# Kernel optimization log

Measured on AMD Instinct MI355X. Metric: run time of the kernel, lower is better.

## Reference

```python
import jax, jax.numpy as jnp
import numpy as np

N, M, DIM = 50000, 800000, 64
EPS_MSG = 1e-7
BN_EPS = 1e-5


def setup_inputs() -> dict:
    key = jax.random.key(0)
    ks = jax.random.split(key, 12)
    x = jax.random.normal(ks[0], (N, DIM), dtype=jnp.float32)
    edge_index = jax.random.randint(ks[1], (2, M), 0, N, dtype=jnp.int64)
    edge_attr = jax.random.normal(ks[2], (M, DIM), dtype=jnp.float32)
    s = 1.0 / np.sqrt(DIM)
    s2 = 1.0 / np.sqrt(2 * DIM)
    # 3 GENConv layers, each with MLP: Linear(dim,2dim)->BN->ReLU->Linear(2dim,dim)
    W1 = jax.random.uniform(ks[3], (3, DIM, 2 * DIM), jnp.float32, -s, s)
    b1 = jax.random.uniform(ks[4], (3, 2 * DIM), jnp.float32, -s, s)
    gamma = jnp.ones((3, 2 * DIM), jnp.float32)
    beta = jnp.zeros((3, 2 * DIM), jnp.float32)
    W2 = jax.random.uniform(ks[5], (3, 2 * DIM, DIM), jnp.float32, -s2, s2)
    b2 = jax.random.uniform(ks[6], (3, DIM), jnp.float32, -s2, s2)
    return {"x": x, "edge_index": edge_index, "edge_attr": edge_attr,
            "W1": W1, "b1": b1, "gamma": gamma, "beta": beta, "W2": W2, "b2": b2}


def _genconv(x, src, dst, edge_attr, W1, b1, g, be, W2, b2):
    n = x.shape[0]
    # message: relu(x_j + e) + eps   (per-edge)
    msg = jax.nn.relu(x[src] + edge_attr) + EPS_MSG  # [M, dim]
    # softmax aggregation (per-destination, per-channel), t=1.0
    mx = jax.ops.segment_max(msg, dst, num_segments=n)
    mx = jnp.where(jnp.isfinite(mx), mx, 0.0)  # empty segments
    e = jnp.exp(msg - mx[dst])
    ssum = jax.ops.segment_sum(e, dst, num_segments=n)
    alpha = e / jnp.maximum(ssum[dst], 1e-16)
    agg = jax.ops.segment_sum(msg * alpha, dst, num_segments=n)  # [N, dim]
    # residual then MLP: Linear -> BatchNorm(train) -> ReLU -> Linear
    h = agg + x
    h1 = h @ W1 + b1
    mu = h1.mean(axis=0)
    var = h1.var(axis=0)
    h1 = (h1 - mu) * jax.lax.rsqrt(var + BN_EPS) * g + be
    h1 = jax.nn.relu(h1)
    return h1 @ W2 + b2


def reference(x, edge_index, edge_attr, W1, b1, gamma, beta, W2, b2):
    src, dst = edge_index[0], edge_index[1]
    for i in range(3):
        x = _genconv(x, src, dst, edge_attr, W1[i], b1[i], gamma[i], beta[i], W2[i], b2[i])
    return x
```

## Files before the change

kernel.cpp:

```cpp
#include <hip/hip_runtime.h>
#include <hip/hip_fp16.h>

#define DIM 64
#define D2  128


__global__ void k_detect(const int* __restrict__ ei, int m, int* __restrict__ flag) {
  __shared__ int nz;
  int t = threadIdx.x;
  if (t == 0) nz = 0;
  __syncthreads();
  int lim = 4096;
  if (lim > m / 2) lim = m / 2;
  int any = 0;
  for (int i = t; i < lim; i += 256) any |= (ei[2 * i + 1] != 0);
  if (any) atomicOr(&nz, 1);
  __syncthreads();
  if (t == 0) flag[0] = nz ? 0 : 1;
}

__global__ void k_hist(const int* __restrict__ ei, int m, const int* __restrict__ flag,
                       int* __restrict__ cnt) {
  int i = blockIdx.x * 256 + threadIdx.x;
  if (i >= m) return;
  int f = flag[0];
  int d = f ? ei[2 * ((size_t)m + i)] : ei[(size_t)m + i];
  atomicAdd(&cnt[d], 1);
}

__global__ void k_scanA(const int* __restrict__ cnt, int* __restrict__ excl,
                        int* __restrict__ bsum, int n) {
  __shared__ int lds[256];
  int t = threadIdx.x;
  int i = blockIdx.x * 256 + t;
  int v = (i < n) ? cnt[i] : 0;
  lds[t] = v;
  __syncthreads();
  for (int off = 1; off < 256; off <<= 1) {
    int u = (t >= off) ? lds[t - off] : 0;
    __syncthreads();
    lds[t] += u;
    __syncthreads();
  }
  if (i < n) excl[i] = lds[t] - v;
  if (t == 255) bsum[blockIdx.x] = lds[255];
}

__global__ void k_scanC(const int* __restrict__ excl, const int* __restrict__ bsum,
                        int* __restrict__ start, int* __restrict__ cursor, int n, int m) {
  __shared__ int red[256];
  __shared__ int boffS;
  int t = threadIdx.x;
  int acc = 0;
  for (int i = t; i < blockIdx.x; i += 256) acc += bsum[i];
  red[t] = acc;
  __syncthreads();
  for (int off = 128; off > 0; off >>= 1) {
    if (t < off) red[t] += red[t + off];
    __syncthreads();
  }
  if (t == 0) boffS = red[0];
  __syncthreads();
  int i = blockIdx.x * 256 + t;
  if (i < n) {
    int s = excl[i] + boffS;
    start[i] = s;
    cursor[i] = s;
  }
  if (blockIdx.x == 0 && t == 0) start[n] = m;
}

__global__ void k_scatter(const int* __restrict__ ei, int m, const int* __restrict__ flag,
                          int* __restrict__ cursor, int2* __restrict__ sed) {
  int i = blockIdx.x * 256 + threadIdx.x;
  if (i >= m) return;
  int f = flag[0];
  int s, d;
  if (f) { s = ei[2 * (size_t)i]; d = ei[2 * ((size_t)m + i)]; }
  else   { s = ei[i];             d = ei[(size_t)m + i]; }
  int pos = atomicAdd(&cursor[d], 1);
  sed[pos] = make_int2(i, s);
}

__global__ __launch_bounds__(256) void k_canon(
    int2* __restrict__ sed, const int* __restrict__ start, int n) {
  int lane = threadIdx.x & 63;
  int node = blockIdx.x * 4 + (threadIdx.x >> 6);
  if (node >= n) return;
  int s0 = start[node], s1 = start[node + 1];

#define BSTEP(K, J)                                   \
  {                                                   \
    int o = __shfl_xor(key, (J), 64);                 \
    bool dir = ((lane & (K)) == 0);                   \
    bool lo = ((lane & (J)) == 0);                    \
    int mn = key < o ? key : o;                       \
    int mx = key < o ? o : key;                       \
    key = (dir == lo) ? mn : mx;                      \
  }

  for (int base = s0; base < s1; base += 64) {
    int cnt = s1 - base;
    if (cnt > 64) cnt = 64;
    int key = 0x7fffffff;
    int srcReg = 0;
    if (lane < cnt) {
      int2 e = sed[base + lane];
      key = (e.x << 6) | lane;
      srcReg = e.y;
    }
#pragma unroll
    for (int k = 2; k <= 16; k <<= 1) {
#pragma unroll
      for (int j = k >> 1; j > 0; j >>= 1) BSTEP(k, j)
    }
    if (cnt > 16) {
#pragma unroll
      for (int j = 16; j > 0; j >>= 1) BSTEP(32, j)
      if (cnt > 32) {
#pragma unroll
        for (int j = 32; j > 0; j >>= 1) BSTEP(64, j)
      }
    }
    int org = key & 63;
    int eid = (int)(((unsigned)key) >> 6);
    int src = __shfl(srcReg, org, 64);
    if (lane < cnt) sed[base + lane] = make_int2(eid, src);
  }
#undef BSTEP
}

__global__ __launch_bounds__(256) void k_perm(
    const float* __restrict__ ea, const int2* __restrict__ sed,
    __half* __restrict__ eah, int m) {
  int cl = threadIdx.x & 15;
  int grp = (blockIdx.x * 256 + threadIdx.x) >> 4;
  int ngrp = (gridDim.x * 256) >> 4;
  for (int p0 = grp * 4; p0 < m; p0 += ngrp * 4) {
#pragma unroll
    for (int k = 0; k < 4; k++) {
      int p = p0 + k;
      if (p < m) {
        int eid = sed[p].x;
        float4 v = *(const float4*)(ea + ((size_t)eid << 6) + (cl << 2));
        __half2 h0 = __floats2half2_rn(v.x, v.y);
        __half2 h1 = __floats2half2_rn(v.z, v.w);
        uint2 u;
        u.x = *(unsigned*)&h0;
        u.y = *(unsigned*)&h1;
        *(uint2*)(eah + (((size_t)p) << 6) + (cl << 2)) = u;
      }
    }
  }
}

__global__ __launch_bounds__(256) void k_agg_s(
    const float* __restrict__ x, const __half* __restrict__ eah,
    const int2* __restrict__ sed, const int* __restrict__ start,
    float* __restrict__ h, int n) {
  int lane = threadIdx.x & 63;
  int node = blockIdx.x * 4 + (threadIdx.x >> 6);
  if (node >= n) return;
  int sub = lane >> 4;
  int cl = lane & 15;
  int s0 = start[node], s1 = start[node + 1];

  float sS[4] = {0.f, 0.f, 0.f, 0.f};
  float wW[4] = {0.f, 0.f, 0.f, 0.f};

#define CONSUME()                                                       \
  {                                                                     \
    float2 a01 = __half22float2(*(const __half2*)&av.x);                \
    float2 a23 = __half22float2(*(const __half2*)&av.y);                \
    float g0 = fmaxf(xv.x + a01.x, 0.f) + 1e-7f;                        \
    float g1 = fmaxf(xv.y + a01.y, 0.f) + 1e-7f;                        \
    float g2 = fmaxf(xv.z + a23.x, 0.f) + 1e-7f;                        \
    float g3 = fmaxf(xv.w + a23.y, 0.f) + 1e-7f;                        \
    float p0 = __expf(g0), p1 = __expf(g1), p2 = __expf(g2), p3 = __expf(g3); \
    sS[0] += p0; sS[1] += p1; sS[2] += p2; sS[3] += p3;                 \
    wW[0] = fmaf(g0, p0, wW[0]); wW[1] = fmaf(g1, p1, wW[1]);           \
    wW[2] = fmaf(g2, p2, wW[2]); wW[3] = fmaf(g3, p3, wW[3]);           \
  }

  for (int base = s0; base < s1; base += 64) {
    int cnt = s1 - base;
    if (cnt > 64) cnt = 64;
    int sK = 0;
    if (lane < cnt) sK = sed[base + lane].y;
    int full = cnt >> 2;
    int rem = cnt & 3;
    int idx = (sub < cnt) ? sub : 0;
    int src = __shfl(sK, idx, 64);
    float4 xv = *(const float4*)(x + ((size_t)src << 6) + (cl << 2));
    uint2 av = *(const uint2*)(eah + (((size_t)(base + idx)) << 6) + (cl << 2));
    for (int t = 0; t < full; t++) {
      int nidx = 4 * t + 4 + sub;
      int nidxc = (nidx < cnt) ? nidx : 0;
      int nsrc = __shfl(sK, nidxc, 64);
      float4 nxv = *(const float4*)(x + ((size_t)nsrc << 6) + (cl << 2));
      uint2 nav = *(const uint2*)(eah + (((size_t)(base + nidxc)) << 6) + (cl << 2));
      CONSUME()
      xv = nxv; av = nav;
    }
    if (rem) {
      if (sub < rem) CONSUME()
    }
  }
#undef CONSUME

#pragma unroll
  for (int off = 16; off < 64; off <<= 1) {
#pragma unroll
    for (int c = 0; c < 4; c++) {
      sS[c] += __shfl_xor(sS[c], off, 64);
      wW[c] += __shfl_xor(wW[c], off, 64);
    }
  }

  if (sub == 0) {
    size_t xo = ((size_t)node << 6) + (cl << 2);
    float4 xv = *(const float4*)(x + xo);
    float4 o;
    o.x = wW[0] / fmaxf(sS[0], 1e-16f) + xv.x;
    o.y = wW[1] / fmaxf(sS[1], 1e-16f) + xv.y;
    o.z = wW[2] / fmaxf(sS[2], 1e-16f) + xv.z;
    o.w = wW[3] / fmaxf(sS[3], 1e-16f) + xv.w;
    *(float4*)(h + xo) = o;
  }
}

__global__ __launch_bounds__(256) void k_agg_g(
    const float* __restrict__ x, const float* __restrict__ ea,
    const int2* __restrict__ sed, const int* __restrict__ start,
    float* __restrict__ h, int n) {
  int lane = threadIdx.x & 63;
  int node = blockIdx.x * 4 + (threadIdx.x >> 6);
  if (node >= n) return;
  int sub = lane >> 4;
  int cl = lane & 15;
  int s0 = start[node], s1 = start[node + 1];

  float sS[4] = {0.f, 0.f, 0.f, 0.f};
  float wW[4] = {0.f, 0.f, 0.f, 0.f};

#define ACC(EID, SRC)                                                   \
  {                                                                     \
    unsigned xo = ((unsigned)(SRC) << 6) + (cl << 2);                   \
    unsigned ao = ((unsigned)(EID) << 6) + (cl << 2);                   \
    float4 xv = *(const float4*)(x + xo);                               \
    float4 av = *(const float4*)(ea + ao);                              \
    float g0 = fmaxf(xv.x + av.x, 0.f) + 1e-7f;                         \
    float g1 = fmaxf(xv.y + av.y, 0.f) + 1e-7f;                         \
    float g2 = fmaxf(xv.z + av.z, 0.f) + 1e-7f;                         \
    float g3 = fmaxf(xv.w + av.w, 0.f) + 1e-7f;                         \
    float p0 = __expf(g0), p1 = __expf(g1), p2 = __expf(g2), p3 = __expf(g3); \
    sS[0] += p0; sS[1] += p1; sS[2] += p2; sS[3] += p3;                 \
    wW[0] = fmaf(g0, p0, wW[0]); wW[1] = fmaf(g1, p1, wW[1]);           \
    wW[2] = fmaf(g2, p2, wW[2]); wW[3] = fmaf(g3, p3, wW[3]);           \
  }

  for (int base = s0; base < s1; base += 64) {
    int cnt = s1 - base;
    if (cnt > 64) cnt = 64;
    int eK = 0, sK = 0;
    if (lane < cnt) {
      int2 e = sed[base + lane];
      eK = e.x; sK = e.y;
    }
    int full = cnt >> 2;
    int rem = cnt & 3;
    for (int t = 0; t < full; t++) {
      int idx = 4 * t + sub;
      int eid = __shfl(eK, idx, 64);
      int src = __shfl(sK, idx, 64);
      ACC(eid, src)
    }
    if (rem) {
      int idx = 4 * full + sub;
      int idxc = idx < cnt ? idx : 0;
      int eid = __shfl(eK, idxc, 64);
      int src = __shfl(sK, idxc, 64);
      if (sub < rem) ACC(eid, src)
    }
  }
#undef ACC

#pragma unroll
  for (int off = 16; off < 64; off <<= 1) {
#pragma unroll
    for (int c = 0; c < 4; c++) {
      sS[c] += __shfl_xor(sS[c], off, 64);
      wW[c] += __shfl_xor(wW[c], off, 64);
    }
  }

  if (sub == 0) {
    unsigned xo = ((unsigned)node << 6) + (cl << 2);
    float4 xv = *(const float4*)(x + xo);
    float4 o;
    o.x = wW[0] / fmaxf(sS[0], 1e-16f) + xv.x;
    o.y = wW[1] / fmaxf(sS[1], 1e-16f) + xv.y;
    o.z = wW[2] / fmaxf(sS[2], 1e-16f) + xv.z;
    o.w = wW[3] / fmaxf(sS[3], 1e-16f) + xv.w;
    *(float4*)(h + xo) = o;
  }
}

__global__ __launch_bounds__(256) void k_gemm1(
    const float* __restrict__ h, const float* __restrict__ W1,
    const float* __restrict__ b1, float* __restrict__ h1,
    float* __restrict__ ps, float* __restrict__ pq, int n) {
  __shared__ float ws[DIM * D2];
  __shared__ float hs[DIM][68];
  __shared__ float red[8][D2];
  int tid = threadIdx.x;
  int row0 = blockIdx.x * 64;
  const float4* w4 = (const float4*)W1;
  float4* ws4 = (float4*)ws;
#pragma unroll
  for (int i = 0; i < 8; i++) ws4[tid + 256 * i] = w4[tid + 256 * i];
  const float4* h4 = (const float4*)h;
#pragma unroll
  for (int i = 0; i < 4; i++) {
    int idx = tid + 256 * i;
    int r = idx & 63, dg = idx >> 6;
    int row = row0 + r;
    float4 v = make_float4(0.f, 0.f, 0.f, 0.f);
    if (row < n) v = h4[(size_t)row * 16 + dg];
    int c = dg * 4;
    hs[c + 0][r] = v.x; hs[c + 1][r] = v.y; hs[c + 2][r] = v.z; hs[c + 3][r] = v.w;
  }
  __syncthreads();

  int tc = tid & 31, tr = tid >> 5;
  float bb[4];
#pragma unroll
  for (int k = 0; k < 4; k++) bb[k] = b1[tc * 4 + k];
  float acc[8][4];
#pragma unroll
  for (int i = 0; i < 8; i++)
#pragma unroll
    for (int k = 0; k < 4; k++) acc[i][k] = bb[k];
#pragma unroll 4
  for (int d = 0; d < DIM; d++) {
    float4 wv = *(const float4*)&ws[d * D2 + tc * 4];
    float4 ha = *(const float4*)&hs[d][tr * 8];
    float4 hb = *(const float4*)&hs[d][tr * 8 + 4];
    float hr[8] = {ha.x, ha.y, ha.z, ha.w, hb.x, hb.y, hb.z, hb.w};
    float wk[4] = {wv.x, wv.y, wv.z, wv.w};
#pragma unroll
    for (int i = 0; i < 8; i++)
#pragma unroll
      for (int k = 0; k < 4; k++) acc[i][k] = fmaf(hr[i], wk[k], acc[i][k]);
  }
  float cs[4] = {0.f, 0.f, 0.f, 0.f}, cq[4] = {0.f, 0.f, 0.f, 0.f};
#pragma unroll
  for (int i = 0; i < 8; i++) {
    int row = row0 + tr * 8 + i;
    if (row < n) {
      ((float4*)h1)[(size_t)row * 32 + tc] =
          make_float4(acc[i][0], acc[i][1], acc[i][2], acc[i][3]);
#pragma unroll
      for (int k = 0; k < 4; k++) { cs[k] += acc[i][k]; cq[k] += acc[i][k] * acc[i][k]; }
    }
  }
  __syncthreads();
#pragma unroll
  for (int k = 0; k < 4; k++) red[tr][tc * 4 + k] = cs[k];
  __syncthreads();
  float asum = 0.f;
  if (tid < D2) {
#pragma unroll
    for (int r = 0; r < 8; r++) asum += red[r][tid];
  }
  __syncthreads();
#pragma unroll
  for (int k = 0; k < 4; k++) red[tr][tc * 4 + k] = cq[k];
  __syncthreads();
  if (tid < D2) {
    float bsumv = 0.f;
#pragma unroll
    for (int r = 0; r < 8; r++) bsumv += red[r][tid];
    ps[(size_t)tid * gridDim.x + blockIdx.x] = asum;
    pq[(size_t)tid * gridDim.x + blockIdx.x] = bsumv;
  }
}

__global__ __launch_bounds__(256) void k_stats(
    const float* __restrict__ ps, const float* __restrict__ pq,
    const float* __restrict__ gamma, const float* __restrict__ beta,
    float* __restrict__ ss, int rows, int n) {
  __shared__ float r0[256], r1[256];
  int j = blockIdx.x;
  int t = threadIdx.x;
  float a = 0.f, b = 0.f;
  for (int r = t; r < rows; r += 256) {
    a += ps[(size_t)j * rows + r];
    b += pq[(size_t)j * rows + r];
  }
  r0[t] = a; r1[t] = b;
  __syncthreads();
  for (int off = 128; off > 0; off >>= 1) {
    if (t < off) { r0[t] += r0[t + off]; r1[t] += r1[t + off]; }
    __syncthreads();
  }
  if (t == 0) {
    float mu = r0[0] / (float)n;
    float var = r1[0] / (float)n - mu * mu;
    float sc = gamma[j] * rsqrtf(var + 1e-5f);
    ss[j] = sc;
    ss[D2 + j] = beta[j] - mu * sc;
  }
}

__global__ __launch_bounds__(256) void k_gemm2(
    const float* __restrict__ h1, const float* __restrict__ W2,
    const float* __restrict__ b2, const float* __restrict__ ss,
    float* __restrict__ out, int n) {
  __shared__ float ws2[D2 * DIM];
  __shared__ float hs[D2][68];
  __shared__ float scS[D2], shS[D2];
  int tid = threadIdx.x;
  int row0 = blockIdx.x * 64;
  const float4* w4 = (const float4*)W2;
  float4* ws4 = (float4*)ws2;
#pragma unroll
  for (int i = 0; i < 8; i++) ws4[tid + 256 * i] = w4[tid + 256 * i];
  if (tid < D2) { scS[tid] = ss[tid]; shS[tid] = ss[D2 + tid]; }
  __syncthreads();
  const float4* h14 = (const float4*)h1;
#pragma unroll
  for (int i = 0; i < 8; i++) {
    int idx = tid + 256 * i;
    int r = idx & 63, cg = idx >> 6;
    int row = row0 + r;
    float4 v = make_float4(0.f, 0.f, 0.f, 0.f);
    if (row < n) v = h14[(size_t)row * 32 + cg];
    int c = cg * 4;
    hs[c + 0][r] = fmaxf(fmaf(v.x, scS[c + 0], shS[c + 0]), 0.f);
    hs[c + 1][r] = fmaxf(fmaf(v.y, scS[c + 1], shS[c + 1]), 0.f);
    hs[c + 2][r] = fmaxf(fmaf(v.z, scS[c + 2], shS[c + 2]), 0.f);
    hs[c + 3][r] = fmaxf(fmaf(v.w, scS[c + 3], shS[c + 3]), 0.f);
  }
  __syncthreads();
  int tc = tid & 15, tr = tid >> 4;
  float bb[4];
#pragma unroll
  for (int k = 0; k < 4; k++) bb[k] = b2[tc * 4 + k];
  float acc[4][4];
#pragma unroll
  for (int i = 0; i < 4; i++)
#pragma unroll
    for (int k = 0; k < 4; k++) acc[i][k] = bb[k];
#pragma unroll 4
  for (int d = 0; d < D2; d++) {
    float4 wv = *(const float4*)&ws2[d * DIM + tc * 4];
    float4 hv = *(const float4*)&hs[d][tr * 4];
    float hr[4] = {hv.x, hv.y, hv.z, hv.w};
    float wk[4] = {wv.x, wv.y, wv.z, wv.w};
#pragma unroll
    for (int i = 0; i < 4; i++)
#pragma unroll
      for (int k = 0; k < 4; k++) acc[i][k] = fmaf(hr[i], wk[k], acc[i][k]);
  }
#pragma unroll
  for (int i = 0; i < 4; i++) {
    int row = row0 + tr * 4 + i;
    if (row < n)
      ((float4*)out)[(size_t)row * 16 + tc] =
          make_float4(acc[i][0], acc[i][1], acc[i][2], acc[i][3]);
  }
}

extern "C" void kernel_launch(void* const* d_in, const int* in_sizes, int n_in,
                              void* d_out, int out_size, void* d_ws, size_t ws_size,
                              hipStream_t stream) {
  (void)n_in; (void)out_size;
  const float* x0    = (const float*)d_in[0];
  const int*   ei    = (const int*)d_in[1];
  const float* ea    = (const float*)d_in[2];
  const float* W1    = (const float*)d_in[3];
  const float* b1    = (const float*)d_in[4];
  const float* gamma = (const float*)d_in[5];
  const float* beta  = (const float*)d_in[6];
  const float* W2    = (const float*)d_in[7];
  const float* b2    = (const float*)d_in[8];
  float* out = (float*)d_out;

  int n = in_sizes[0] / DIM;
  int m = in_sizes[1] / 2;

  char* base = (char*)d_ws;
  size_t off = 0;
  auto alloc = [&](size_t bytes) -> void* {
    void* p = base + off;
    off += (bytes + 255) & ~(size_t)255;
    return p;
  };
  int*    cnt    = (int*)alloc((size_t)n * 4);
  int*    excl   = (int*)alloc((size_t)n * 4);
  int*    bsum   = (int*)alloc(256 * 4);
  int*    start  = (int*)alloc((size_t)(n + 1) * 4);
  int*    cursor = (int*)alloc((size_t)n * 4);
  int*    flag   = (int*)alloc(256);
  int2*   sed    = (int2*)alloc((size_t)m * 8);
  float*  h      = (float*)alloc((size_t)n * DIM * 4);
  float*  h1     = (float*)alloc((size_t)n * D2 * 4);
  int tiles = (n + 63) / 64;
  float* ps = (float*)alloc((size_t)tiles * D2 * 4);
  float* pq = (float*)alloc((size_t)tiles * D2 * 4);
  float* ss = (float*)alloc(256 * 4);
  size_t eah_bytes = (size_t)m * DIM * 2;
  __half* eah = nullptr;
  if (ws_size >= off + eah_bytes) eah = (__half*)alloc(eah_bytes);

  hipMemsetAsync(cnt, 0, (size_t)n * 4, stream);
  k_detect<<<1, 256, 0, stream>>>(ei, m, flag);
  int mg = (m + 255) / 256;
  int ng = (n + 255) / 256;
  int ag = (n + 3) / 4;
  k_hist<<<mg, 256, 0, stream>>>(ei, m, flag, cnt);
  k_scanA<<<ng, 256, 0, stream>>>(cnt, excl, bsum, n);
  k_scanC<<<ng, 256, 0, stream>>>(excl, bsum, start, cursor, n, m);
  k_scatter<<<mg, 256, 0, stream>>>(ei, m, flag, cursor, sed);
  k_canon<<<ag, 256, 0, stream>>>(sed, start, n);
  if (eah) k_perm<<<2048, 256, 0, stream>>>(ea, sed, eah, m);

  for (int l = 0; l < 3; l++) {
    const float* xin = (l == 0) ? x0 : out;
    if (eah) k_agg_s<<<ag, 256, 0, stream>>>(xin, eah, sed, start, h, n);
    else     k_agg_g<<<ag, 256, 0, stream>>>(xin, ea,  sed, start, h, n);
    k_gemm1<<<tiles, 256, 0, stream>>>(h, W1 + (size_t)l * DIM * D2, b1 + (size_t)l * D2,
                                       h1, ps, pq, n);
    k_stats<<<D2, 256, 0, stream>>>(ps, pq, gamma + (size_t)l * D2, beta + (size_t)l * D2,
                                    ss, tiles, n);
    k_gemm2<<<tiles, 256, 0, stream>>>(h1, W2 + (size_t)l * D2 * DIM, b2 + (size_t)l * DIM,
                                       ss, out, n);
  }
}
```

Baseline: 714.9 us.

## Gather fp16 node features in aggregation and scatter-permute edge attrs via inverse

Keeps a half-precision copy of the node features, produced by a conversion kernel for layer 0 and written by gemm2 for later layers. The aggregation kernel gathers these fp16 rows instead of fp32, halving the random-gather traffic. The edge-attribute permutation now reads edge attributes sequentially and scatters writes through a computed inverse permutation, replacing the previous random reads. This adds extra fp16 writes, an inverse-index kernel and reduced precision on the x_j path.

```diff
diff --git a/kernel.cpp b/kernel.cpp
--- a/kernel.cpp
+++ b/kernel.cpp
@@ -130,34 +130,54 @@
 #undef BSTEP
 }
 
-__global__ __launch_bounds__(256) void k_perm(
-    const float* __restrict__ ea, const int2* __restrict__ sed,
+__global__ void k_inv(const int2* __restrict__ sed, int* __restrict__ inv, int m) {
+  int i = blockIdx.x * 256 + threadIdx.x;
+  if (i < m) inv[sed[i].x] = i;
+}
+
+__global__ __launch_bounds__(256) void k_perm2(
+    const float* __restrict__ ea, const int* __restrict__ inv,
     __half* __restrict__ eah, int m) {
   int cl = threadIdx.x & 15;
   int grp = (blockIdx.x * 256 + threadIdx.x) >> 4;
   int ngrp = (gridDim.x * 256) >> 4;
-  for (int p0 = grp * 4; p0 < m; p0 += ngrp * 4) {
+  for (int e0 = grp * 4; e0 < m; e0 += ngrp * 4) {
 #pragma unroll
     for (int k = 0; k < 4; k++) {
-      int p = p0 + k;
-      if (p < m) {
-        int eid = sed[p].x;
+      int eid = e0 + k;
+      if (eid < m) {
+        int pos = inv[eid];
         float4 v = *(const float4*)(ea + ((size_t)eid << 6) + (cl << 2));
         __half2 h0 = __floats2half2_rn(v.x, v.y);
         __half2 h1 = __floats2half2_rn(v.z, v.w);
         uint2 u;
         u.x = *(unsigned*)&h0;
         u.y = *(unsigned*)&h1;
-        *(uint2*)(eah + (((size_t)p) << 6) + (cl << 2)) = u;
+        *(uint2*)(eah + (((size_t)pos) << 6) + (cl << 2)) = u;
       }
     }
   }
 }
 
+__global__ void k_half(const float* __restrict__ x, __half* __restrict__ xh, int total8) {
+  int i = blockIdx.x * 256 + threadIdx.x;
+  if (i >= total8) return;
+  float4 a = ((const float4*)x)[2 * i];
+  float4 b = ((const float4*)x)[2 * i + 1];
+  __half2 h0 = __floats2half2_rn(a.x, a.y);
+  __half2 h1 = __floats2half2_rn(a.z, a.w);
+  __half2 h2 = __floats2half2_rn(b.x, b.y);
+  __half2 h3 = __floats2half2_rn(b.z, b.w);
+  uint4 u;
+  u.x = *(unsigned*)&h0; u.y = *(unsigned*)&h1;
+  u.z = *(unsigned*)&h2; u.w = *(unsigned*)&h3;
+  ((uint4*)xh)[i] = u;
+}
+
 __global__ __launch_bounds__(256) void k_agg_s(
-    const float* __restrict__ x, const __half* __restrict__ eah,
-    const int2* __restrict__ sed, const int* __restrict__ start,
-    float* __restrict__ h, int n) {
+    const float* __restrict__ x, const __half* __restrict__ xh,
+    const __half* __restrict__ eah, const int2* __restrict__ sed,
+    const int* __restrict__ start, float* __restrict__ h, int n) {
   int lane = threadIdx.x & 63;
   int node = blockIdx.x * 4 + (threadIdx.x >> 6);
   if (node >= n) return;
@@ -170,12 +190,14 @@
 
 #define CONSUME()                                                       \
   {                                                                     \
+    float2 x01 = __half22float2(*(const __half2*)&xu.x);                \
+    float2 x23 = __half22float2(*(const __half2*)&xu.y);                \
     float2 a01 = __half22float2(*(const __half2*)&av.x);                \
     float2 a23 = __half22float2(*(const __half2*)&av.y);                \
-    float g0 = fmaxf(xv.x + a01.x, 0.f) + 1e-7f;                        \
-    float g1 = fmaxf(xv.y + a01.y, 0.f) + 1e-7f;                        \
-    float g2 = fmaxf(xv.z + a23.x, 0.f) + 1e-7f;                        \
-    float g3 = fmaxf(xv.w + a23.y, 0.f) + 1e-7f;                        \
+    float g0 = fmaxf(x01.x + a01.x, 0.f) + 1e-7f;                       \
+    float g1 = fmaxf(x01.y + a01.y, 0.f) + 1e-7f;                       \
+    float g2 = fmaxf(x23.x + a23.x, 0.f) + 1e-7f;                       \
+    float g3 = fmaxf(x23.y + a23.y, 0.f) + 1e-7f;                       \
     float p0 = __expf(g0), p1 = __expf(g1), p2 = __expf(g2), p3 = __expf(g3); \
     sS[0] += p0; sS[1] += p1; sS[2] += p2; sS[3] += p3;                 \
     wW[0] = fmaf(g0, p0, wW[0]); wW[1] = fmaf(g1, p1, wW[1]);           \
@@ -191,16 +213,16 @@
     int rem = cnt & 3;
     int idx = (sub < cnt) ? sub : 0;
     int src = __shfl(sK, idx, 64);
-    float4 xv = *(const float4*)(x + ((size_t)src << 6) + (cl << 2));
+    uint2 xu = *(const uint2*)(xh + ((size_t)src << 6) + (cl << 2));
     uint2 av = *(const uint2*)(eah + (((size_t)(base + idx)) << 6) + (cl << 2));
     for (int t = 0; t < full; t++) {
       int nidx = 4 * t + 4 + sub;
       int nidxc = (nidx < cnt) ? nidx : 0;
       int nsrc = __shfl(sK, nidxc, 64);
-      float4 nxv = *(const float4*)(x + ((size_t)nsrc << 6) + (cl << 2));
+      uint2 nxu = *(const uint2*)(xh + ((size_t)nsrc << 6) + (cl << 2));
       uint2 nav = *(const uint2*)(eah + (((size_t)(base + nidxc)) << 6) + (cl << 2));
       CONSUME()
-      xv = nxv; av = nav;
+      xu = nxu; av = nav;
     }
     if (rem) {
       if (sub < rem) CONSUME()
@@ -416,7 +438,7 @@
 __global__ __launch_bounds__(256) void k_gemm2(
     const float* __restrict__ h1, const float* __restrict__ W2,
     const float* __restrict__ b2, const float* __restrict__ ss,
-    float* __restrict__ out, int n) {
+    float* __restrict__ out, __half* __restrict__ xh, int n) {
   __shared__ float ws2[D2 * DIM];
   __shared__ float hs[D2][68];
   __shared__ float scS[D2], shS[D2];
@@ -466,9 +488,18 @@
 #pragma unroll
   for (int i = 0; i < 4; i++) {
     int row = row0 + tr * 4 + i;
-    if (row < n)
+    if (row < n) {
       ((float4*)out)[(size_t)row * 16 + tc] =
           make_float4(acc[i][0], acc[i][1], acc[i][2], acc[i][3]);
+      if (xh) {
+        __half2 p0 = __floats2half2_rn(acc[i][0], acc[i][1]);
+        __half2 p1 = __floats2half2_rn(acc[i][2], acc[i][3]);
+        uint2 u;
+        u.x = *(unsigned*)&p0;
+        u.y = *(unsigned*)&p1;
+        *(uint2*)(xh + (size_t)row * DIM + tc * 4) = u;
+      }
+    }
   }
 }
 
@@ -510,6 +541,8 @@
   float* ps = (float*)alloc((size_t)tiles * D2 * 4);
   float* pq = (float*)alloc((size_t)tiles * D2 * 4);
   float* ss = (float*)alloc(256 * 4);
+  __half* xh  = (__half*)alloc((size_t)n * DIM * 2);
+  int*    inv = (int*)alloc((size_t)m * 4);
   size_t eah_bytes = (size_t)m * DIM * 2;
   __half* eah = nullptr;
   if (ws_size >= off + eah_bytes) eah = (__half*)alloc(eah_bytes);
@@ -524,17 +557,21 @@
   k_scanC<<<ng, 256, 0, stream>>>(excl, bsum, start, cursor, n, m);
   k_scatter<<<mg, 256, 0, stream>>>(ei, m, flag, cursor, sed);
   k_canon<<<ag, 256, 0, stream>>>(sed, start, n);
-  if (eah) k_perm<<<2048, 256, 0, stream>>>(ea, sed, eah, m);
+  if (eah) {
+    k_inv<<<mg, 256, 0, stream>>>(sed, inv, m);
+    k_perm2<<<2048, 256, 0, stream>>>(ea, inv, eah, m);
+    k_half<<<(n * DIM / 8 + 255) / 256, 256, 0, stream>>>(x0, xh, n * DIM / 8);
+  }
 
   for (int l = 0; l < 3; l++) {
     const float* xin = (l == 0) ? x0 : out;
-    if (eah) k_agg_s<<<ag, 256, 0, stream>>>(xin, eah, sed, start, h, n);
-    else     k_agg_g<<<ag, 256, 0, stream>>>(xin, ea,  sed, start, h, n);
+    if (eah) k_agg_s<<<ag, 256, 0, stream>>>(xin, xh, eah, sed, start, h, n);
+    else     k_agg_g<<<ag, 256, 0, stream>>>(xin, ea, sed, start, h, n);
     k_gemm1<<<tiles, 256, 0, stream>>>(h, W1 + (size_t)l * DIM * D2, b1 + (size_t)l * D2,
                                        h1, ps, pq, n);
     k_stats<<<D2, 256, 0, stream>>>(ps, pq, gamma + (size_t)l * D2, beta + (size_t)l * D2,
                                     ss, tiles, n);
     k_gemm2<<<tiles, 256, 0, stream>>>(h1, W2 + (size_t)l * D2 * DIM, b2 + (size_t)l * DIM,
-                                       ss, out, n);
-  }
-}
+                                       ss, out, eah ? xh : nullptr, n);
+  }
+}
```

New measurement: 706.5 us. Within noise of the previous version (-1.2%).
